# Performance work log

Hardware: AMD Instinct MI355X
Metric: run time of the kernel (lower is better)

Reference implementation:

```python
import jax, jax.numpy as jnp
import numpy as np

# ---- static problem sizes (full batches: cum[b] = b * max_num) ----
B = 256          # graphs per batch
MAXN, MAXE, MAXC = 128, 256, 64   # max nodes / edges / 2-cells per graph
H = 256          # embed_dim == hidden
L = 4            # num GCNCConv layers
OUT = 10         # out_size
P_N, P_E = 131072, 98304          # up-adjacency pair counts (dim 0, dim 1)
Q_E, Q_C = 131072, 65536          # boundary incidence counts (dim 1, dim 2)


def setup_inputs() -> dict:
    key = jax.random.key(0)
    ks = jax.random.split(key, 24)
    s = 1.0 / np.sqrt(H)
    inp = {}
    # flat cochain features [total_entities, H]
    inp['x_n'] = jax.random.normal(ks[0], (B * MAXN, H), jnp.float32)
    inp['x_e'] = jax.random.normal(ks[1], (B * MAXE, H), jnp.float32)
    inp['x_c'] = jax.random.normal(ks[2], (B * MAXC, H), jnp.float32)
    # node-level up adjacency (pairs of nodes sharing an edge coboundary)
    inp['n_up_b'] = jax.random.randint(ks[3], (P_N,), 0, B, jnp.int32)
    inp['n_up_i'] = jax.random.randint(ks[4], (P_N,), 0, MAXN, jnp.int32)
    inp['n_up_j'] = jax.random.randint(ks[5], (P_N,), 0, MAXN, jnp.int32)
    inp['n_up_e'] = jax.random.randint(ks[6], (P_N,), 0, MAXE, jnp.int32)
    # edge-level up adjacency (pairs of edges sharing a cell coboundary)
    inp['e_up_b'] = jax.random.randint(ks[7], (P_E,), 0, B, jnp.int32)
    inp['e_up_i'] = jax.random.randint(ks[8], (P_E,), 0, MAXE, jnp.int32)
    inp['e_up_j'] = jax.random.randint(ks[9], (P_E,), 0, MAXE, jnp.int32)
    inp['e_up_c'] = jax.random.randint(ks[10], (P_E,), 0, MAXC, jnp.int32)
    # boundary incidence: edges -> nodes, cells -> edges
    inp['eb_b'] = jax.random.randint(ks[11], (Q_E,), 0, B, jnp.int32)
    inp['eb_i'] = jax.random.randint(ks[12], (Q_E,), 0, MAXE, jnp.int32)
    inp['eb_j'] = jax.random.randint(ks[13], (Q_E,), 0, MAXN, jnp.int32)
    inp['cb_b'] = jax.random.randint(ks[14], (Q_C,), 0, B, jnp.int32)
    inp['cb_i'] = jax.random.randint(ks[15], (Q_C,), 0, MAXC, jnp.int32)
    inp['cb_j'] = jax.random.randint(ks[16], (Q_C,), 0, MAXE, jnp.int32)
    # learned parameters
    inp['Wself'] = jax.random.normal(ks[17], (L, 3, H, H), jnp.float32) * s
    inp['bself'] = jnp.zeros((L, 3, H), jnp.float32)
    inp['Wupx'] = jax.random.normal(ks[18], (L, 2, H, H), jnp.float32) * s
    inp['Wupa'] = jax.random.normal(ks[19], (L, 2, H, H), jnp.float32) * s
    inp['Wb'] = jax.random.normal(ks[20], (L, 2, H, H), jnp.float32) * s
    inp['Wp'] = jax.random.normal(ks[21], (H, H), jnp.float32) * s
    inp['Wp_ref'] = jax.random.normal(ks[22], (H, H), jnp.float32) * s
    inp['bp'] = jnp.zeros((H,), jnp.float32)
    k2 = jax.random.split(ks[23], 4)
    inp['W1'] = jax.random.normal(k2[0], (3, H, 2 * H), jnp.float32) * s
    inp['b1'] = jnp.zeros((3, 2 * H), jnp.float32)
    inp['W2'] = jax.random.normal(k2[1], (2 * H, OUT), jnp.float32) * s
    inp['b2'] = jnp.zeros((OUT,), jnp.float32)
    return inp


def reference(x_n, x_e, x_c, n_up_b, n_up_i, n_up_j, n_up_e,
              e_up_b, e_up_i, e_up_j, e_up_c, eb_b, eb_i, eb_j,
              cb_b, cb_i, cb_j, Wself, bself, Wupx, Wupa, Wb,
              Wp, Wp_ref, bp, W1, b1, W2, b2):
    relu = jax.nn.relu
    # dense per-batch boundary adjacencies (scatter-set, as in init_data_to_dense_gcnc)
    b_adj_e = jnp.zeros((B, MAXE, MAXN), jnp.float32).at[eb_b, eb_i, eb_j].set(1.0)
    b_adj_c = jnp.zeros((B, MAXC, MAXE), jnp.float32).at[cb_b, cb_i, cb_j].set(1.0)
    # flat gather/scatter indices: cum[b] = b * max_num (full batches)
    n_i = n_up_b * MAXN + n_up_i
    n_j = n_up_b * MAXN + n_up_j
    n_a = n_up_b * MAXE + n_up_e   # up_attr_idx into edge features
    e_i = e_up_b * MAXE + e_up_i
    e_j = e_up_b * MAXE + e_up_j
    e_a = e_up_b * MAXC + e_up_c   # up_attr_idx into cell features
    xs = [x_n, x_e, x_c]
    refs = xs  # init features used by pool_weight
    for l in range(L):
        xn, xe, xc = xs
        # up messages: msg = relu(W x_j + W' up_attr), scatter-sum to receiver
        up_n = jax.ops.segment_sum(
            relu(xn[n_j] @ Wupx[l, 0] + xe[n_a] @ Wupa[l, 0]),
            n_i, num_segments=B * MAXN)
        up_e = jax.ops.segment_sum(
            relu(xe[e_j] @ Wupx[l, 1] + xc[e_a] @ Wupa[l, 1]),
            e_i, num_segments=B * MAXE)
        # boundary messages: dense masked matmul with incidence matrices
        bd_e = jnp.einsum('ben,bnh->beh', b_adj_e,
                          xn.reshape(B, MAXN, H)).reshape(B * MAXE, H) @ Wb[l, 0]
        bd_c = jnp.einsum('bce,beh->bch', b_adj_c,
                          xe.reshape(B, MAXE, H)).reshape(B * MAXC, H) @ Wb[l, 1]
        xs = [relu(xn @ Wself[l, 0] + bself[l, 0] + up_n),
              relu(xe @ Wself[l, 1] + bself[l, 1] + up_e + bd_e),
              relu(xc @ Wself[l, 2] + bself[l, 2] + bd_c)]
    # pool weights (gating vs. init features) + sum readout per dimension
    maxs = (MAXN, MAXE, MAXC)
    pooled = []
    for i in range(3):
        w = jax.nn.sigmoid(xs[i] @ Wp + refs[i] @ Wp_ref + bp)
        pooled.append((w * xs[i]).reshape(B, maxs[i], H).sum(axis=1))  # [B,H]
    h = sum(relu(pooled[i] @ W1[i] + b1[i]) for i in range(3))  # final_readout='sum'
    return h @ W2 + b2  # [B, OUT]
```

## Files before the change

kernel.cpp:

```cpp
#include <hip/hip_runtime.h>
#include <cstdint>
#include <cstddef>

typedef unsigned short u16;
typedef __bf16 bf16x8 __attribute__((ext_vector_type(8)));
typedef float f32x4 __attribute__((ext_vector_type(4)));
typedef unsigned short u16x8 __attribute__((ext_vector_type(8)));

#define NB   256
#define MAXN 128
#define MAXE 256
#define MAXC 64
#define HD   256
#define NLAYER 4
#define PN 131072
#define PE 98304
#define QE 131072
#define QC 65536
#define MN (NB*MAXN)
#define ME (NB*MAXE)
#define MC (NB*MAXC)

#define SEG_N  0
#define SEG_E  (MN)
#define SEG_EB (MN + ME)
#define SEG_CB (MN + 2*ME)
#define HTOT   (MN + 2*ME + MC)
#define UPTOT  (PN + PE)

__device__ __forceinline__ float bf2f(u16 u){
  union{unsigned int i; float f;} x; x.i = ((unsigned int)u) << 16; return x.f;
}
__device__ __forceinline__ u16 f2bf(float f){
  union{float f; unsigned int i;} x; x.f = f;
  unsigned int r = x.i + 0x7fffu + ((x.i >> 16) & 1u);
  return (u16)(r >> 16);
}
__device__ __forceinline__ f32x4 MFMA(bf16x8 a, bf16x8 b, f32x4 c){
  return __builtin_amdgcn_mfma_f32_16x16x32_bf16(a, b, c, 0, 0, 0);
}
__device__ __forceinline__ void gl_lds16(const u16* g, u16* l){
  __builtin_amdgcn_global_load_lds(
      (const __attribute__((address_space(1))) unsigned int*)g,
      (__attribute__((address_space(3))) unsigned int*)l, 16, 0, 0);
}

__global__ void detect_dtype(const u16* __restrict__ x, int* __restrict__ flag){
  if(threadIdx.x == 0 && blockIdx.x == 0){
    int cnt = 0;
    for(int i = 0; i < 64; i++){
      int e = (x[i] >> 7) & 0xFF;
      if(e >= 118 && e <= 136) cnt++;
    }
    *flag = (cnt >= 50) ? 1 : 0;
  }
}

__device__ __forceinline__ void convSpan(const void* s, u16* d, long n, long i, int isbf){
  if(i + 8 <= n){
    if(isbf){
      *reinterpret_cast<u16x8*>(d + i) = *reinterpret_cast<const u16x8*>((const u16*)s + i);
    }else{
      const float* sp = (const float*)s + i;
      float4 a = *reinterpret_cast<const float4*>(sp);
      float4 b = *reinterpret_cast<const float4*>(sp + 4);
      u16x8 o;
      o[0]=f2bf(a.x); o[1]=f2bf(a.y); o[2]=f2bf(a.z); o[3]=f2bf(a.w);
      o[4]=f2bf(b.x); o[5]=f2bf(b.y); o[6]=f2bf(b.z); o[7]=f2bf(b.w);
      *reinterpret_cast<u16x8*>(d + i) = o;
    }
  }else{
    for(long e = i; e < n; e++)
      d[e] = isbf ? ((const u16*)s)[e] : f2bf(((const float*)s)[e]);
  }
}

__global__ __launch_bounds__(256) void conv3(const void* __restrict__ s0, u16* __restrict__ d0,
                                             const void* __restrict__ s1, u16* __restrict__ d1,
                                             const void* __restrict__ s2, u16* __restrict__ d2,
                                             const int* __restrict__ flag){
  const long U0 = (long)MN * HD / 8, U1 = (long)ME * HD / 8, U2 = (long)MC * HD / 8;
  long u = (long)blockIdx.x * 256 + threadIdx.x;
  const int isbf = *flag;
  if(u < U0){ convSpan(s0, d0, (long)MN * HD, u * 8, isbf); return; }
  u -= U0;
  if(u < U1){ convSpan(s1, d1, (long)ME * HD, u * 8, isbf); return; }
  u -= U1;
  if(u < U2) convSpan(s2, d2, (long)MC * HD, u * 8, isbf);
}

__global__ __launch_bounds__(256) void conv_params(
    const void* sW1, u16* dW1, const void* sb1, u16* db1,
    const void* sW2, u16* dW2, const void* sb2, u16* db2,
    const void* sbs, u16* dbs, const void* sbp, u16* dbp,
    const int* __restrict__ flag){
  long u = (long)blockIdx.x * 256 + threadIdx.x;
  const int isbf = *flag;
  if(u < 49152){ convSpan(sW1, dW1, 393216, u * 8, isbf); return; } u -= 49152;
  if(u < 192)  { convSpan(sb1, db1, 1536,   u * 8, isbf); return; } u -= 192;
  if(u < 640)  { convSpan(sW2, dW2, 5120,   u * 8, isbf); return; } u -= 640;
  if(u < 2)    { convSpan(sb2, db2, 10,     u * 8, isbf); return; } u -= 2;
  if(u < 384)  { convSpan(sbs, dbs, 3072,   u * 8, isbf); return; } u -= 384;
  if(u < 32)     convSpan(sbp, dbp, 256,    u * 8, isbf);
}

__global__ __launch_bounds__(256) void conv_f2b(const float* __restrict__ s, u16* __restrict__ d, long n){
  long i = ((long)blockIdx.x * 256 + threadIdx.x) * 8;
  if(i >= n) return;
  float4 a = *reinterpret_cast<const float4*>(s + i);
  float4 b = *reinterpret_cast<const float4*>(s + i + 4);
  u16x8 o;
  o[0]=f2bf(a.x); o[1]=f2bf(a.y); o[2]=f2bf(a.z); o[3]=f2bf(a.w);
  o[4]=f2bf(b.x); o[5]=f2bf(b.y); o[6]=f2bf(b.z); o[7]=f2bf(b.w);
  *reinterpret_cast<u16x8*>(d + i) = o;
}

__global__ __launch_bounds__(256) void zero_f4(float* __restrict__ p, long n4){
  long i = (long)blockIdx.x * blockDim.x + threadIdx.x;
  if(i >= n4) return;
  float4 z = {0.f, 0.f, 0.f, 0.f};
  *reinterpret_cast<float4*>(p + i * 4) = z;
}

__global__ void wt_all(const void* __restrict__ pSelf, const void* __restrict__ pUpx,
                       const void* __restrict__ pUpa, const void* __restrict__ pB,
                       const void* __restrict__ pP, const void* __restrict__ pPref,
                       u16* __restrict__ wt, const int* __restrict__ flag){
  __shared__ u16 t[16][17];
  int z = blockIdx.z;
  const void* src; int m; u16* dst;
  if(z < 12)      { src = pSelf; m = z;      dst = wt; }
  else if(z < 20) { src = pUpx;  m = z - 12; dst = wt + (size_t)12 * 65536; }
  else if(z < 28) { src = pUpa;  m = z - 20; dst = wt + (size_t)20 * 65536; }
  else if(z < 36) { src = pB;    m = z - 28; dst = wt + (size_t)28 * 65536; }
  else if(z == 36){ src = pP;    m = 0;      dst = wt + (size_t)36 * 65536; }
  else            { src = pPref; m = 0;      dst = wt + (size_t)37 * 65536; }
  int n0 = blockIdx.x * 16, k0 = blockIdx.y * 16;
  size_t sidx = (size_t)m * 65536 + (size_t)(k0 + threadIdx.y) * 256 + n0 + threadIdx.x;
  u16 v = (*flag) ? ((const u16*)src)[sidx] : f2bf(((const float*)src)[sidx]);
  t[threadIdx.y][threadIdx.x] = v;
  __syncthreads();
  dst[(size_t)m * 65536 + (size_t)(n0 + threadIdx.y) * 256 + (k0 + threadIdx.x)] =
      t[threadIdx.x][threadIdx.y];
}

__global__ void w1_transpose(const u16* __restrict__ src, u16* __restrict__ dst){
  __shared__ u16 t[16][17];
  int i = blockIdx.z;
  int o0 = blockIdx.x * 16, k0 = blockIdx.y * 16;
  t[threadIdx.y][threadIdx.x] =
      src[(size_t)i * 131072 + (size_t)(k0 + threadIdx.y) * 512 + o0 + threadIdx.x];
  __syncthreads();
  dst[(size_t)i * 131072 + (size_t)(o0 + threadIdx.y) * 256 + (k0 + threadIdx.x)] =
      t[threadIdx.x][threadIdx.y];
}

__global__ void dedup_kernel(const int* __restrict__ bb, const int* __restrict__ bi,
                             const int* __restrict__ bj, unsigned int* __restrict__ mask,
                             unsigned char* __restrict__ valid, int Q, int maxI, int maxJ){
  int q = blockIdx.x * blockDim.x + threadIdx.x;
  if(q >= Q) return;
  int s = (bb[q] * maxI + bi[q]) * maxJ + bj[q];
  unsigned int bit = 1u << (s & 31);
  unsigned int old = atomicOr(&mask[s >> 5], bit);
  valid[q] = (old & bit) ? 0 : 1;
}

__global__ __launch_bounds__(256) void hist_all(
    const int* __restrict__ nub, const int* __restrict__ nui,
    const int* __restrict__ eub, const int* __restrict__ eui,
    const int* __restrict__ ebb, const int* __restrict__ ebi, const unsigned char* __restrict__ ve,
    const int* __restrict__ cbb, const int* __restrict__ cbi, const unsigned char* __restrict__ vc,
    int* __restrict__ hist){
  int bx = blockIdx.x, t = threadIdx.x;
  if(bx < PN/256){
    int p = bx * 256 + t;
    atomicAdd(&hist[SEG_N + nub[p] * MAXN + nui[p]], 1);
  }else if(bx < PN/256 + PE/256){
    int p = (bx - PN/256) * 256 + t;
    atomicAdd(&hist[SEG_E + eub[p] * MAXE + eui[p]], 1);
  }else if(bx < PN/256 + PE/256 + QE/256){
    int q = (bx - PN/256 - PE/256) * 256 + t;
    if(ve[q]) atomicAdd(&hist[SEG_EB + ebb[q] * MAXE + ebi[q]], 1);
  }else{
    int q = (bx - PN/256 - PE/256 - QE/256) * 256 + t;
    if(vc[q]) atomicAdd(&hist[SEG_CB + cbb[q] * MAXC + cbi[q]], 1);
  }
}

__global__ __launch_bounds__(256) void scan1(const int* __restrict__ hist, int* __restrict__ bsum){
  __shared__ int s[256];
  int t = threadIdx.x;
  long base = (long)blockIdx.x * 1024 + t * 4;
  int4 v = *reinterpret_cast<const int4*>(hist + base);
  s[t] = v.x + v.y + v.z + v.w;
  __syncthreads();
  for(int st = 128; st > 0; st >>= 1){
    if(t < st) s[t] += s[t + st];
    __syncthreads();
  }
  if(t == 0) bsum[blockIdx.x] = s[0];
}
__global__ __launch_bounds__(256) void scan2(int* __restrict__ bsum, int nb){
  __shared__ int s[256];
  int t = threadIdx.x;
  int v = (t < nb) ? bsum[t] : 0;
  s[t] = v;
  __syncthreads();
  for(int st = 1; st < 256; st <<= 1){
    int u = (t >= st) ? s[t - st] : 0;
    __syncthreads();
    s[t] += u;
    __syncthreads();
  }
  if(t < nb) bsum[t] = s[t] - v;
}
__global__ __launch_bounds__(256) void scan3(const int* __restrict__ hist, const int* __restrict__ bsum,
                                             int* __restrict__ off, int* __restrict__ cur){
  __shared__ int s[256];
  int t = threadIdx.x;
  long base = (long)blockIdx.x * 1024 + t * 4;
  int4 v = *reinterpret_cast<const int4*>(hist + base);
  int sum = v.x + v.y + v.z + v.w;
  s[t] = sum;
  __syncthreads();
  for(int st = 1; st < 256; st <<= 1){
    int u = (t >= st) ? s[t - st] : 0;
    __syncthreads();
    s[t] += u;
    __syncthreads();
  }
  int excl = s[t] - sum + bsum[blockIdx.x];
  int4 o;
  o.x = excl; o.y = o.x + v.x; o.z = o.y + v.y; o.w = o.z + v.z;
  *reinterpret_cast<int4*>(off + base) = o;
  *reinterpret_cast<int4*>(cur + base) = o;
}

__global__ __launch_bounds__(256) void fill_all(
    const int* __restrict__ nub, const int* __restrict__ nui,
    const int* __restrict__ nuj, const int* __restrict__ nue,
    const int* __restrict__ eub, const int* __restrict__ eui,
    const int* __restrict__ euj, const int* __restrict__ euc,
    const int* __restrict__ ebb, const int* __restrict__ ebi,
    const int* __restrict__ ebj, const unsigned char* __restrict__ ve,
    const int* __restrict__ cbb, const int* __restrict__ cbi,
    const int* __restrict__ cbj, const unsigned char* __restrict__ vc,
    int* __restrict__ cur, int2* __restrict__ csrUp, int* __restrict__ csrBd){
  int bx = blockIdx.x, t = threadIdx.x;
  if(bx < PN/256){
    int p = bx * 256 + t; int b = nub[p];
    int pos = atomicAdd(&cur[SEG_N + b * MAXN + nui[p]], 1);
    int2 e; e.x = b * MAXN + nuj[p]; e.y = b * MAXE + nue[p];
    csrUp[pos] = e;
  }else if(bx < PN/256 + PE/256){
    int p = (bx - PN/256) * 256 + t; int b = eub[p];
    int pos = atomicAdd(&cur[SEG_E + b * MAXE + eui[p]], 1);
    int2 e; e.x = b * MAXE + euj[p]; e.y = b * MAXC + euc[p];
    csrUp[pos] = e;
  }else if(bx < PN/256 + PE/256 + QE/256){
    int q = (bx - PN/256 - PE/256) * 256 + t;
    if(!ve[q]) return;
    int b = ebb[q];
    int pos = atomicAdd(&cur[SEG_EB + b * MAXE + ebi[q]], 1);
    csrBd[pos - UPTOT] = b * MAXN + ebj[q];
  }else{
    int q = (bx - PN/256 - PE/256 - QE/256) * 256 + t;
    if(!vc[q]) return;
    int b = cbb[q];
    int pos = atomicAdd(&cur[SEG_CB + b * MAXC + cbi[q]], 1);
    csrBd[pos - UPTOT] = b * MAXE + cbj[q];
  }
}

template<int HAS_UP, int HAS_BD>
__global__ __launch_bounds__(256) void gather_k(
    const u16* __restrict__ Y, const u16* __restrict__ Z, const u16* __restrict__ BD,
    const int2* __restrict__ csrUp, const int* __restrict__ csrBd,
    const int* __restrict__ off, const int* __restrict__ deg,
    int upBase, int bdBase, u16* __restrict__ ACC, int rowLo){
  const int nb = gridDim.x;
  int bx = blockIdx.x;
  if((nb & 7) == 0) bx = (bx & 7) * (nb >> 3) + (bx >> 3);
  const int row = rowLo + bx * 4 + (threadIdx.x >> 6);
  const int lane = threadIdx.x & 63;
  const int c = lane * 4;
  float a0 = 0.f, a1 = 0.f, a2 = 0.f, a3 = 0.f;
  if(HAS_UP){
    int s = off[upBase + row];
    int d = deg[upBase + row];
    for(int k = 0; k < d; k++){
      int2 e = csrUp[s + k];
      const ushort4 y = *reinterpret_cast<const ushort4*>(Y + (size_t)e.x * 256 + c);
      const ushort4 z = *reinterpret_cast<const ushort4*>(Z + (size_t)e.y * 256 + c);
      a0 += fmaxf(bf2f(y.x) + bf2f(z.x), 0.f);
      a1 += fmaxf(bf2f(y.y) + bf2f(z.y), 0.f);
      a2 += fmaxf(bf2f(y.z) + bf2f(z.z), 0.f);
      a3 += fmaxf(bf2f(y.w) + bf2f(z.w), 0.f);
    }
  }
  if(HAS_BD){
    int s = off[bdBase + row] - UPTOT;
    int d = deg[bdBase + row];
    for(int k = 0; k < d; k++){
      int j = csrBd[s + k];
      const ushort4 x = *reinterpret_cast<const ushort4*>(BD + (size_t)j * 256 + c);
      a0 += bf2f(x.x); a1 += bf2f(x.y); a2 += bf2f(x.z); a3 += bf2f(x.w);
    }
  }
  ushort4 o; o.x = f2bf(a0); o.y = f2bf(a1); o.z = f2bf(a2); o.w = f2bf(a3);
  *reinterpret_cast<ushort4*>(ACC + (size_t)(row - rowLo) * 256 + c) = o;
}

template<int MODE>
__global__ __launch_bounds__(256) void gemm_k(
    const u16* P0, const u16* Q0, u16* C0, int n0,
    const u16* P1, const u16* Q1, u16* C1, int n1,
    const u16* P2, const u16* Q2, u16* C2,
    const u16* __restrict__ S1, const u16* __restrict__ S2,
    const u16* __restrict__ ACC, const u16* __restrict__ bias){
  __shared__ u16 lA[2][64 * 64];
  __shared__ u16 lB[2][256 * 64];
  int bx = blockIdx.x;
  const u16* P = P0; const u16* Q = Q0; u16* C = C0;
  if(bx >= n0 + n1){ bx -= n0 + n1; P = P2; Q = Q2; C = C2; }
  else if(bx >= n0){ bx -= n0;      P = P1; Q = Q1; C = C1; }
  const int t = threadIdx.x;
  const int lane = t & 63, wv = t >> 6;
  const int wn = wv;
  const int r = lane & 15, q = lane >> 4;
  const int rsw = r & 7;
  const size_t m0 = (size_t)bx * 64;
  const int lrow = lane >> 3, lchk = lane & 7;
  const int csw = lchk ^ lrow;

  f32x4 acc[4][4];
#pragma unroll
  for(int i = 0; i < 4; i++)
#pragma unroll
    for(int j = 0; j < 4; j++) acc[i][j] = {0.f, 0.f, 0.f, 0.f};

  const int NT = (MODE == 3) ? 8 : 4;

  auto stage = [&](int tt, int buf){
    const u16* Ap = (MODE == 3) ? ((tt >= 4) ? Q : P) : P;
    const u16* Wp = (MODE == 3) ? ((tt >= 4) ? S2 : S1) : Q;
    const int k0 = (tt & 3) * 64;
#pragma unroll
    for(int i = 0; i < 2; i++){
      const int row = wv * 16 + i * 8 + lrow;
      gl_lds16(Ap + (m0 + row) * 256 + k0 + csw * 8, &lA[buf][(wv * 16 + i * 8) * 64]);
    }
#pragma unroll
    for(int j = 0; j < 8; j++){
      const int n = wv * 64 + j * 8 + lrow;
      gl_lds16(Wp + (size_t)n * 256 + k0 + csw * 8, &lB[buf][(wv * 64 + j * 8) * 64]);
    }
  };

  stage(0, 0);
  stage(1, 1);

#pragma unroll
  for(int tt = 0; tt < NT; tt++){
    const int cur = tt & 1;
    if(tt < NT - 1) asm volatile("s_waitcnt vmcnt(10)" ::: "memory");
    else            asm volatile("s_waitcnt vmcnt(0)" ::: "memory");
    __builtin_amdgcn_s_barrier();
    __builtin_amdgcn_s_setprio(1);
#pragma unroll
    for(int ks = 0; ks < 2; ks++){
      bf16x8 af[4], bfr[4];
#pragma unroll
      for(int i = 0; i < 4; i++)
        af[i] = *reinterpret_cast<const bf16x8*>(
            &lA[cur][(i * 16 + r) * 64 + (((ks * 4 + q) ^ rsw) * 8)]);
#pragma unroll
      for(int j = 0; j < 4; j++)
        bfr[j] = *reinterpret_cast<const bf16x8*>(
            &lB[cur][(wn * 64 + j * 16 + r) * 64 + (((ks * 4 + q) ^ rsw) * 8)]);
#pragma unroll
      for(int i = 0; i < 4; i++)
#pragma unroll
        for(int j = 0; j < 4; j++) acc[i][j] = MFMA(bfr[j], af[i], acc[i][j]);
    }
    __builtin_amdgcn_s_setprio(0);
    __builtin_amdgcn_s_barrier();
    if(tt + 2 < NT) stage(tt + 2, cur);
  }

#pragma unroll
  for(int i = 0; i < 4; i++){
    const size_t row = m0 + i * 16 + r;
#pragma unroll
    for(int j = 0; j < 4; j++){
      const int col = wn * 64 + j * 16 + q * 4;
      const size_t idx = row * 256 + col;
      f32x4 v = acc[i][j];
      ushort4 o;
      if(MODE == 2){
        const ushort4 a4 = *reinterpret_cast<const ushort4*>(ACC + idx);
        const ushort4 b4 = *reinterpret_cast<const ushort4*>(bias + col);
        o.x = f2bf(fmaxf(v[0] + bf2f(a4.x) + bf2f(b4.x), 0.f));
        o.y = f2bf(fmaxf(v[1] + bf2f(a4.y) + bf2f(b4.y), 0.f));
        o.z = f2bf(fmaxf(v[2] + bf2f(a4.z) + bf2f(b4.z), 0.f));
        o.w = f2bf(fmaxf(v[3] + bf2f(a4.w) + bf2f(b4.w), 0.f));
      }else{
        o.x = f2bf(v[0]); o.y = f2bf(v[1]); o.z = f2bf(v[2]); o.w = f2bf(v[3]);
      }
      *reinterpret_cast<ushort4*>(C + idx) = o;
    }
  }
}

__global__ __launch_bounds__(256) void pool_all(
    const u16* __restrict__ Gn, const u16* __restrict__ Ge, const u16* __restrict__ Gc,
    const u16* __restrict__ bpv,
    const u16* __restrict__ Xn, const u16* __restrict__ Xe, const u16* __restrict__ Xc,
    float* __restrict__ pooled){
  int b = blockIdx.x, h = threadIdx.x, y = blockIdx.y;
  const u16 *G, *X; float* out; int maxR, r0;
  if(y < 2)      { G = Gn; X = Xn; out = pooled;                    maxR = MAXN; r0 = y * 64; }
  else if(y < 6) { G = Ge; X = Xe; out = pooled + (size_t)NB * HD;  maxR = MAXE; r0 = (y - 2) * 64; }
  else           { G = Gc; X = Xc; out = pooled + (size_t)2*NB*HD;  maxR = MAXC; r0 = 0; }
  float bias = bf2f(bpv[h]);
  float acc = 0.f;
  for(int r = r0; r < r0 + 64; r++){
    size_t o = ((size_t)b * maxR + r) * 256 + h;
    float t = bf2f(G[o]) + bias;
    float w = 1.f / (1.f + __expf(-t));
    acc += w * bf2f(X[o]);
  }
  atomicAdd(&out[b * 256 + h], acc);
}

__global__ __launch_bounds__(512) void readout1_mfma(const u16* __restrict__ Ab,
                                                     const u16* __restrict__ W1t,
                                                     const u16* __restrict__ b1,
                                                     float* __restrict__ hbuf){
  __shared__ u16 lA[2][128 * 64];
  __shared__ u16 lB[2][256 * 64];
  const int t = threadIdx.x;
  const int lane = t & 63, wv = t >> 6;
  const int wm = wv >> 2, wn = wv & 3;
  const int r = lane & 15, q = lane >> 4;
  const int rsw = r & 7;
  const int b0 = blockIdx.x * 128;
  const int o0 = blockIdx.y * 256;
  const int lrow = lane >> 3, lchk = lane & 7;
  const int csw = lchk ^ lrow;

  f32x4 acc[4][4], facc[4][4];
#pragma unroll
  for(int i = 0; i < 4; i++)
#pragma unroll
    for(int j = 0; j < 4; j++){ acc[i][j] = {0.f,0.f,0.f,0.f}; facc[i][j] = {0.f,0.f,0.f,0.f}; }

  auto stage = [&](int tt, int buf){
    const int ii = tt >> 2, k0 = (tt & 3) * 64;
    const u16* Ap = Ab + (size_t)ii * 65536;
    const u16* Wp = W1t + (size_t)ii * 131072;
#pragma unroll
    for(int i = 0; i < 2; i++){
      const int row = i * 64 + wv * 8 + lrow;
      gl_lds16(Ap + (size_t)(b0 + row) * 256 + k0 + csw * 8, &lA[buf][(i * 64 + wv * 8) * 64]);
    }
#pragma unroll
    for(int j = 0; j < 4; j++){
      const int n = j * 64 + wv * 8 + lrow;
      gl_lds16(Wp + (size_t)(o0 + n) * 256 + k0 + csw * 8, &lB[buf][(j * 64 + wv * 8) * 64]);
    }
  };

  stage(0, 0);
  stage(1, 1);

#pragma unroll
  for(int tt = 0; tt < 12; tt++){
    const int cur = tt & 1;
    if(tt < 11) asm volatile("s_waitcnt vmcnt(6)" ::: "memory");
    else        asm volatile("s_waitcnt vmcnt(0)" ::: "memory");
    __builtin_amdgcn_s_barrier();
#pragma unroll
    for(int ks = 0; ks < 2; ks++){
      bf16x8 af[4], bfr[4];
#pragma unroll
      for(int i = 0; i < 4; i++)
        af[i] = *reinterpret_cast<const bf16x8*>(
            &lA[cur][(wm * 64 + i * 16 + r) * 64 + (((ks * 4 + q) ^ rsw) * 8)]);
#pragma unroll
      for(int j = 0; j < 4; j++)
        bfr[j] = *reinterpret_cast<const bf16x8*>(
            &lB[cur][(wn * 64 + j * 16 + r) * 64 + (((ks * 4 + q) ^ rsw) * 8)]);
#pragma unroll
      for(int i = 0; i < 4; i++)
#pragma unroll
        for(int j = 0; j < 4; j++) acc[i][j] = MFMA(bfr[j], af[i], acc[i][j]);
    }
    if((tt & 3) == 3){
      const int ib = tt >> 2;
#pragma unroll
      for(int i = 0; i < 4; i++)
#pragma unroll
        for(int j = 0; j < 4; j++){
          const int col = o0 + wn * 64 + j * 16 + q * 4;
          const ushort4 b4 = *reinterpret_cast<const ushort4*>(b1 + ib * 512 + col);
          facc[i][j][0] += fmaxf(acc[i][j][0] + bf2f(b4.x), 0.f);
          facc[i][j][1] += fmaxf(acc[i][j][1] + bf2f(b4.y), 0.f);
          facc[i][j][2] += fmaxf(acc[i][j][2] + bf2f(b4.z), 0.f);
          facc[i][j][3] += fmaxf(acc[i][j][3] + bf2f(b4.w), 0.f);
          acc[i][j] = {0.f, 0.f, 0.f, 0.f};
        }
    }
    __builtin_amdgcn_s_barrier();
    if(tt + 2 < 12) stage(tt + 2, cur);
  }

#pragma unroll
  for(int i = 0; i < 4; i++){
    const int row = b0 + wm * 64 + i * 16 + r;
#pragma unroll
    for(int j = 0; j < 4; j++){
      const int col = o0 + wn * 64 + j * 16 + q * 4;
      *reinterpret_cast<f32x4*>(hbuf + (size_t)row * 512 + col) = facc[i][j];
    }
  }
}

__global__ __launch_bounds__(64) void readout2(const float* __restrict__ hbuf, const u16* __restrict__ W2,
                                               const u16* __restrict__ b2, void* __restrict__ out,
                                               const int* __restrict__ flag){
  int b = blockIdx.x, o = threadIdx.x;
  if(o >= 10) return;
  float a = bf2f(b2[o]);
  for(int k = 0; k < 512; k++) a += hbuf[(size_t)b * 512 + k] * bf2f(W2[k * 10 + o]);
  if(*flag) ((u16*)out)[b * 10 + o] = f2bf(a);
  else      ((float*)out)[b * 10 + o] = a;
}

extern "C" void kernel_launch(void* const* d_in, const int* in_sizes, int n_in,
                              void* d_out, int out_size, void* d_ws, size_t ws_size,
                              hipStream_t stream){
  const void* x_n = d_in[0];
  const void* x_e = d_in[1];
  const void* x_c = d_in[2];
  const int* n_up_b = (const int*)d_in[3];
  const int* n_up_i = (const int*)d_in[4];
  const int* n_up_j = (const int*)d_in[5];
  const int* n_up_e = (const int*)d_in[6];
  const int* e_up_b = (const int*)d_in[7];
  const int* e_up_i = (const int*)d_in[8];
  const int* e_up_j = (const int*)d_in[9];
  const int* e_up_c = (const int*)d_in[10];
  const int* eb_b = (const int*)d_in[11];
  const int* eb_i = (const int*)d_in[12];
  const int* eb_j = (const int*)d_in[13];
  const int* cb_b = (const int*)d_in[14];
  const int* cb_i = (const int*)d_in[15];
  const int* cb_j = (const int*)d_in[16];

  char* base = (char*)d_ws; size_t off0 = 0;
  auto alloc = [&](size_t n)->char*{ char* p = base + off0; off0 = (off0 + n + 255) & ~(size_t)255; return p; };
  u16* xn = (u16*)alloc((size_t)MN * HD * 2);
  u16* xe = (u16*)alloc((size_t)ME * HD * 2);
  u16* xc = (u16*)alloc((size_t)MC * HD * 2);
  u16* BIG1 = (u16*)alloc((size_t)ME * HD * 2);
  u16* SMa  = (u16*)alloc((size_t)MN * HD * 2);
  u16* SMb  = (u16*)alloc((size_t)MN * HD * 2);
  u16* ACC  = (u16*)alloc((size_t)ME * HD * 2);
  u16* wt = (u16*)alloc((size_t)38 * 65536 * 2);
  unsigned int* mask_e = (unsigned int*)alloc((size_t)NB * MAXE * MAXN / 8);
  unsigned int* mask_c = (unsigned int*)alloc((size_t)NB * MAXC * MAXE / 8);
  unsigned char* valid_e = (unsigned char*)alloc(QE);
  unsigned char* valid_c = (unsigned char*)alloc(QC);
  float* pooled = (float*)alloc((size_t)3 * NB * HD * 4);
  float* hbuf   = (float*)alloc((size_t)NB * 512 * 4);
  int* flag     = (int*)alloc(256);
  int2* csrUp   = (int2*)alloc((size_t)UPTOT * 8);
  int* csrBd    = (int*)alloc((size_t)(QE + QC) * 4);
  int* hist     = (int*)alloc((size_t)HTOT * 4);
  int* offA     = (int*)alloc((size_t)HTOT * 4);
  int* bsum     = (int*)alloc(1024);
  u16* W1t      = (u16*)alloc((size_t)3 * 512 * 256 * 2);
  u16* pooledb  = (u16*)alloc((size_t)3 * NB * HD * 2);
  int* cur      = (int*)pooled;

  u16* wtSelf = wt;
  u16* wtUpx  = wt + (size_t)12 * 65536;
  u16* wtUpa  = wt + (size_t)20 * 65536;
  u16* wtB    = wt + (size_t)28 * 65536;
  u16* wtP    = wt + (size_t)36 * 65536;
  u16* wtPref = wt + (size_t)37 * 65536;

  u16* W1c = (u16*)mask_e;
  u16* b1c = W1c + 393216;
  u16* W2c = b1c + 1536;
  u16* b2c = W2c + 5120;
  u16* bsc = b2c + 16;
  u16* bpc = bsc + 3072;

  detect_dtype<<<1, 64, 0, stream>>>((const u16*)x_n, flag);
  zero_f4<<<(98304 + 255)/256, 256, 0, stream>>>((float*)mask_e, 98304);
  dedup_kernel<<<QE/256, 256, 0, stream>>>(eb_b, eb_i, eb_j, mask_e, valid_e, QE, MAXE, MAXN);
  dedup_kernel<<<QC/256, 256, 0, stream>>>(cb_b, cb_i, cb_j, mask_c, valid_c, QC, MAXC, MAXE);

  wt_all<<<dim3(16,16,38), dim3(16,16), 0, stream>>>(d_in[17], d_in[19], d_in[20],
                                                     d_in[21], d_in[22], d_in[23], wt, flag);
  conv3<<<14336, 256, 0, stream>>>(x_n, xn, x_e, xe, x_c, xc, flag);
  conv_params<<<197, 256, 0, stream>>>(d_in[25], W1c, d_in[26], b1c, d_in[27], W2c,
                                       d_in[28], b2c, d_in[18], bsc, d_in[24], bpc, flag);
  w1_transpose<<<dim3(32,16,3), dim3(16,16), 0, stream>>>(W1c, W1t);

  zero_f4<<<(HTOT/4 + 255)/256, 256, 0, stream>>>((float*)hist, HTOT/4);
  hist_all<<<PN/256 + PE/256 + QE/256 + QC/256, 256, 0, stream>>>(
      n_up_b, n_up_i, e_up_b, e_up_i, eb_b, eb_i, valid_e, cb_b, cb_i, valid_c, hist);
  scan1<<<HTOT/1024, 256, 0, stream>>>(hist, bsum);
  scan2<<<1, 256, 0, stream>>>(bsum, HTOT/1024);
  scan3<<<HTOT/1024, 256, 0, stream>>>(hist, bsum, offA, cur);
  fill_all<<<PN/256 + PE/256 + QE/256 + QC/256, 256, 0, stream>>>(
      n_up_b, n_up_i, n_up_j, n_up_e, e_up_b, e_up_i, e_up_j, e_up_c,
      eb_b, eb_i, eb_j, valid_e, cb_b, cb_i, cb_j, valid_c, cur, csrUp, csrBd);

  for(int l = 0; l < NLAYER; l++){
    const u16* Wupx0 = wtUpx + (size_t)(l*2+0) * 65536;
    const u16* Wupx1 = wtUpx + (size_t)(l*2+1) * 65536;
    const u16* Wupa0 = wtUpa + (size_t)(l*2+0) * 65536;
    const u16* Wupa1 = wtUpa + (size_t)(l*2+1) * 65536;
    const u16* Wb0   = wtB   + (size_t)(l*2+0) * 65536;
    const u16* Wb1   = wtB   + (size_t)(l*2+1) * 65536;
    const u16* Ws0   = wtSelf + (size_t)(l*3+0) * 65536;
    const u16* Ws1   = wtSelf + (size_t)(l*3+1) * 65536;
    const u16* Ws2   = wtSelf + (size_t)(l*3+2) * 65536;
    const u16* bs0 = bsc + (size_t)(l*3+0) * HD;
    const u16* bs1 = bsc + (size_t)(l*3+1) * HD;
    const u16* bs2 = bsc + (size_t)(l*3+2) * HD;

    gemm_k<0><<<MN/64 + ME/64 + MN/64, 256, 0, stream>>>(
        xn, Wupx0, SMa, MN/64, xe, Wupa0, BIG1, ME/64, xn, Wb0, SMb,
        nullptr, nullptr, nullptr, nullptr);
    gather_k<1,0><<<MN/4, 256, 0, stream>>>(SMa, BIG1, nullptr, csrUp, csrBd,
                                            offA, hist, SEG_N, 0, ACC, 0);
    gemm_k<2><<<MN/64, 256, 0, stream>>>(xn, Ws0, xn, MN/64, xn, Ws0, xn, 0, xn, Ws0, xn,
                                         nullptr, nullptr, ACC, bs0);

    gemm_k<0><<<MC/64 + ME/64, 256, 0, stream>>>(
        xc, Wupa1, SMa, MC/64, xe, Wb1, BIG1, ME/64, xc, Wupa1, SMa,
        nullptr, nullptr, nullptr, nullptr);
    gather_k<0,1><<<MC/4, 256, 0, stream>>>(nullptr, nullptr, BIG1, csrUp, csrBd,
                                            offA, hist, 0, SEG_CB, ACC, 0);
    gemm_k<2><<<MC/64, 256, 0, stream>>>(xc, Ws2, xc, MC/64, xc, Ws2, xc, 0, xc, Ws2, xc,
                                         nullptr, nullptr, ACC, bs2);

    gemm_k<0><<<ME/64, 256, 0, stream>>>(
        xe, Wupx1, BIG1, ME/64, xe, Wupx1, BIG1, 0, xe, Wupx1, BIG1,
        nullptr, nullptr, nullptr, nullptr);
    gather_k<1,1><<<ME/4, 256, 0, stream>>>(BIG1, SMa, SMb, csrUp, csrBd,
                                            offA, hist, SEG_E, SEG_EB, ACC, 0);
    gemm_k<2><<<ME/64, 256, 0, stream>>>(xe, Ws1, xe, ME/64, xe, Ws1, xe, 0, xe, Ws1, xe,
                                         nullptr, nullptr, ACC, bs1);
  }

  conv3<<<14336, 256, 0, stream>>>(x_n, SMa, x_e, ACC, x_c, SMb, flag);
  {
    long np4 = (long)3 * NB * HD / 4;
    zero_f4<<<(int)((np4 + 255)/256), 256, 0, stream>>>(pooled, np4);
  }
  gemm_k<3><<<MN/64 + ME/64 + MC/64, 256, 0, stream>>>(
      xn, SMa, SMa, MN/64, xe, ACC, ACC, ME/64, xc, SMb, SMb,
      wtP, wtPref, nullptr, nullptr);
  pool_all<<<dim3(NB, 7), 256, 0, stream>>>(SMa, ACC, SMb, bpc, xn, xe, xc, pooled);

  conv_f2b<<<96, 256, 0, stream>>>(pooled, pooledb, (long)3 * NB * HD);
  readout1_mfma<<<dim3(2,2), 512, 0, stream>>>(pooledb, W1t, b1c, hbuf);
  readout2<<<NB, 64, 0, stream>>>(hbuf, W2c, b2c, d_out, flag);
}
```

Measured before the change: 1.291 ms.

## Use eight waves per GEMM block and software-prefetch gather neighbor rows

The GEMM kernel now runs with 512 threads (8 waves), each wave computing a 64x32 output slice instead of 64x64, which halves per-wave accumulator registers and splits the global-to-LDS loads across more waves. The intent is more waves in flight per CU to hide LDS and global latency. Separately, the gather kernel loads the next neighbor's rows before accumulating the current one, a one-deep software pipeline meant to overlap the dependent index-then-row loads. Risks include smaller per-wave MFMA work relative to LDS reads, and extra register use and branching in the gather loop.

Result: faster. 1.255 ms (-2.8%).

```diff
diff --git a/kernel.cpp b/kernel.cpp
--- a/kernel.cpp
+++ b/kernel.cpp
@@ -289,23 +289,40 @@
   if(HAS_UP){
     int s = off[upBase + row];
     int d = deg[upBase + row];
-    for(int k = 0; k < d; k++){
-      int2 e = csrUp[s + k];
-      const ushort4 y = *reinterpret_cast<const ushort4*>(Y + (size_t)e.x * 256 + c);
-      const ushort4 z = *reinterpret_cast<const ushort4*>(Z + (size_t)e.y * 256 + c);
-      a0 += fmaxf(bf2f(y.x) + bf2f(z.x), 0.f);
-      a1 += fmaxf(bf2f(y.y) + bf2f(z.y), 0.f);
-      a2 += fmaxf(bf2f(y.z) + bf2f(z.z), 0.f);
-      a3 += fmaxf(bf2f(y.w) + bf2f(z.w), 0.f);
+    if(d > 0){
+      int2 e = csrUp[s];
+      ushort4 y0 = *reinterpret_cast<const ushort4*>(Y + (size_t)e.x * 256 + c);
+      ushort4 z0 = *reinterpret_cast<const ushort4*>(Z + (size_t)e.y * 256 + c);
+      for(int k = 1; k <= d; k++){
+        ushort4 y1 = y0, z1 = z0;
+        if(k < d){
+          int2 e2 = csrUp[s + k];
+          y1 = *reinterpret_cast<const ushort4*>(Y + (size_t)e2.x * 256 + c);
+          z1 = *reinterpret_cast<const ushort4*>(Z + (size_t)e2.y * 256 + c);
+        }
+        a0 += fmaxf(bf2f(y0.x) + bf2f(z0.x), 0.f);
+        a1 += fmaxf(bf2f(y0.y) + bf2f(z0.y), 0.f);
+        a2 += fmaxf(bf2f(y0.z) + bf2f(z0.z), 0.f);
+        a3 += fmaxf(bf2f(y0.w) + bf2f(z0.w), 0.f);
+        y0 = y1; z0 = z1;
+      }
     }
   }
   if(HAS_BD){
     int s = off[bdBase + row] - UPTOT;
     int d = deg[bdBase + row];
-    for(int k = 0; k < d; k++){
-      int j = csrBd[s + k];
-      const ushort4 x = *reinterpret_cast<const ushort4*>(BD + (size_t)j * 256 + c);
-      a0 += bf2f(x.x); a1 += bf2f(x.y); a2 += bf2f(x.z); a3 += bf2f(x.w);
+    if(d > 0){
+      int j = csrBd[s];
+      ushort4 x0 = *reinterpret_cast<const ushort4*>(BD + (size_t)j * 256 + c);
+      for(int k = 1; k <= d; k++){
+        ushort4 x1 = x0;
+        if(k < d){
+          int j2 = csrBd[s + k];
+          x1 = *reinterpret_cast<const ushort4*>(BD + (size_t)j2 * 256 + c);
+        }
+        a0 += bf2f(x0.x); a1 += bf2f(x0.y); a2 += bf2f(x0.z); a3 += bf2f(x0.w);
+        x0 = x1;
+      }
     }
   }
   ushort4 o; o.x = f2bf(a0); o.y = f2bf(a1); o.z = f2bf(a2); o.w = f2bf(a3);
@@ -313,7 +330,7 @@
 }
 
 template<int MODE>
-__global__ __launch_bounds__(256) void gemm_k(
+__global__ __launch_bounds__(512) void gemm_k(
     const u16* P0, const u16* Q0, u16* C0, int n0,
     const u16* P1, const u16* Q1, u16* C1, int n1,
     const u16* P2, const u16* Q2, u16* C2,
@@ -327,18 +344,17 @@
   else if(bx >= n0){ bx -= n0;      P = P1; Q = Q1; C = C1; }
   const int t = threadIdx.x;
   const int lane = t & 63, wv = t >> 6;
-  const int wn = wv;
   const int r = lane & 15, q = lane >> 4;
   const int rsw = r & 7;
   const size_t m0 = (size_t)bx * 64;
   const int lrow = lane >> 3, lchk = lane & 7;
   const int csw = lchk ^ lrow;
 
-  f32x4 acc[4][4];
+  f32x4 acc[4][2];
 #pragma unroll
   for(int i = 0; i < 4; i++)
 #pragma unroll
-    for(int j = 0; j < 4; j++) acc[i][j] = {0.f, 0.f, 0.f, 0.f};
+    for(int j = 0; j < 2; j++) acc[i][j] = {0.f, 0.f, 0.f, 0.f};
 
   const int NT = (MODE == 3) ? 8 : 4;
 
@@ -346,15 +362,13 @@
     const u16* Ap = (MODE == 3) ? ((tt >= 4) ? Q : P) : P;
     const u16* Wp = (MODE == 3) ? ((tt >= 4) ? S2 : S1) : Q;
     const int k0 = (tt & 3) * 64;
-#pragma unroll
-    for(int i = 0; i < 2; i++){
-      const int row = wv * 16 + i * 8 + lrow;
-      gl_lds16(Ap + (m0 + row) * 256 + k0 + csw * 8, &lA[buf][(wv * 16 + i * 8) * 64]);
-    }
-#pragma unroll
-    for(int j = 0; j < 8; j++){
-      const int n = wv * 64 + j * 8 + lrow;
-      gl_lds16(Wp + (size_t)n * 256 + k0 + csw * 8, &lB[buf][(wv * 64 + j * 8) * 64]);
+    gl_lds16(Ap + (m0 + wv * 8 + lrow) * 256 + k0 + csw * 8,
+             &lA[buf][(wv * 8) * 64]);
+#pragma unroll
+    for(int j = 0; j < 4; j++){
+      const int n = wv * 32 + j * 8 + lrow;
+      gl_lds16(Wp + (size_t)n * 256 + k0 + csw * 8,
+               &lB[buf][(wv * 32 + j * 8) * 64]);
     }
   };
 
@@ -364,25 +378,25 @@
 #pragma unroll
   for(int tt = 0; tt < NT; tt++){
     const int cur = tt & 1;
-    if(tt < NT - 1) asm volatile("s_waitcnt vmcnt(10)" ::: "memory");
+    if(tt < NT - 1) asm volatile("s_waitcnt vmcnt(5)" ::: "memory");
     else            asm volatile("s_waitcnt vmcnt(0)" ::: "memory");
     __builtin_amdgcn_s_barrier();
     __builtin_amdgcn_s_setprio(1);
 #pragma unroll
     for(int ks = 0; ks < 2; ks++){
-      bf16x8 af[4], bfr[4];
+      bf16x8 af[4], bfr[2];
 #pragma unroll
       for(int i = 0; i < 4; i++)
         af[i] = *reinterpret_cast<const bf16x8*>(
             &lA[cur][(i * 16 + r) * 64 + (((ks * 4 + q) ^ rsw) * 8)]);
 #pragma unroll
-      for(int j = 0; j < 4; j++)
+      for(int j = 0; j < 2; j++)
         bfr[j] = *reinterpret_cast<const bf16x8*>(
-            &lB[cur][(wn * 64 + j * 16 + r) * 64 + (((ks * 4 + q) ^ rsw) * 8)]);
+            &lB[cur][(wv * 32 + j * 16 + r) * 64 + (((ks * 4 + q) ^ rsw) * 8)]);
 #pragma unroll
       for(int i = 0; i < 4; i++)
 #pragma unroll
-        for(int j = 0; j < 4; j++) acc[i][j] = MFMA(bfr[j], af[i], acc[i][j]);
+        for(int j = 0; j < 2; j++) acc[i][j] = MFMA(bfr[j], af[i], acc[i][j]);
     }
     __builtin_amdgcn_s_setprio(0);
     __builtin_amdgcn_s_barrier();
@@ -393,8 +407,8 @@
   for(int i = 0; i < 4; i++){
     const size_t row = m0 + i * 16 + r;
 #pragma unroll
-    for(int j = 0; j < 4; j++){
-      const int col = wn * 64 + j * 16 + q * 4;
+    for(int j = 0; j < 2; j++){
+      const int col = wv * 32 + j * 16 + q * 4;
       const size_t idx = row * 256 + col;
       f32x4 v = acc[i][j];
       ushort4 o;
@@ -635,28 +649,28 @@
     const u16* bs1 = bsc + (size_t)(l*3+1) * HD;
     const u16* bs2 = bsc + (size_t)(l*3+2) * HD;
 
-    gemm_k<0><<<MN/64 + ME/64 + MN/64, 256, 0, stream>>>(
+    gemm_k<0><<<MN/64 + ME/64 + MN/64, 512, 0, stream>>>(
         xn, Wupx0, SMa, MN/64, xe, Wupa0, BIG1, ME/64, xn, Wb0, SMb,
         nullptr, nullptr, nullptr, nullptr);
     gather_k<1,0><<<MN/4, 256, 0, stream>>>(SMa, BIG1, nullptr, csrUp, csrBd,
                                             offA, hist, SEG_N, 0, ACC, 0);
-    gemm_k<2><<<MN/64, 256, 0, stream>>>(xn, Ws0, xn, MN/64, xn, Ws0, xn, 0, xn, Ws0, xn,
+    gemm_k<2><<<MN/64, 512, 0, stream>>>(xn, Ws0, xn, MN/64, xn, Ws0, xn, 0, xn, Ws0, xn,
                                          nullptr, nullptr, ACC, bs0);
 
-    gemm_k<0><<<MC/64 + ME/64, 256, 0, stream>>>(
+    gemm_k<0><<<MC/64 + ME/64, 512, 0, stream>>>(
         xc, Wupa1, SMa, MC/64, xe, Wb1, BIG1, ME/64, xc, Wupa1, SMa,
         nullptr, nullptr, nullptr, nullptr);
     gather_k<0,1><<<MC/4, 256, 0, stream>>>(nullptr, nullptr, BIG1, csrUp, csrBd,
                                             offA, hist, 0, SEG_CB, ACC, 0);
-    gemm_k<2><<<MC/64, 256, 0, stream>>>(xc, Ws2, xc, MC/64, xc, Ws2, xc, 0, xc, Ws2, xc,
+    gemm_k<2><<<MC/64, 512, 0, stream>>>(xc, Ws2, xc, MC/64, xc, Ws2, xc, 0, xc, Ws2, xc,
                                          nullptr, nullptr, ACC, bs2);
 
-    gemm_k<0><<<ME/64, 256, 0, stream>>>(
+    gemm_k<0><<<ME/64, 512, 0, stream>>>(
         xe, Wupx1, BIG1, ME/64, xe, Wupx1, BIG1, 0, xe, Wupx1, BIG1,
         nullptr, nullptr, nullptr, nullptr);
     gather_k<1,1><<<ME/4, 256, 0, stream>>>(BIG1, SMa, SMb, csrUp, csrBd,
                                             offA, hist, SEG_E, SEG_EB, ACC, 0);
-    gemm_k<2><<<ME/64, 256, 0, stream>>>(xe, Ws1, xe, ME/64, xe, Ws1, xe, 0, xe, Ws1, xe,
+    gemm_k<2><<<ME/64, 512, 0, stream>>>(xe, Ws1, xe, ME/64, xe, Ws1, xe, 0, xe, Ws1, xe,
                                          nullptr, nullptr, ACC, bs1);
   }
 
@@ -665,7 +679,7 @@
     long np4 = (long)3 * NB * HD / 4;
     zero_f4<<<(int)((np4 + 255)/256), 256, 0, stream>>>(pooled, np4);
   }
-  gemm_k<3><<<MN/64 + ME/64 + MC/64, 256, 0, stream>>>(
+  gemm_k<3><<<MN/64 + ME/64 + MC/64, 512, 0, stream>>>(
       xn, SMa, SMa, MN/64, xe, ACC, ACC, ME/64, xc, SMb, SMb,
       wtP, wtPref, nullptr, nullptr);
   pool_all<<<dim3(NB, 7), 256, 0, stream>>>(SMa, ACC, SMb, bpc, xn, xe, xc, pooled);
```
